# Optimization experiments

Hardware: AMD Instinct MI355X
Metric: run time of the kernel (lower is better)

## Reference

```python
import jax, jax.numpy as jnp
import numpy as np

ATTEN = 8  # atten_size -> window W = 2*ATTEN+1 = 17


def setup_inputs() -> dict:
    key = jax.random.key(0)
    ks = jax.random.split(key, 9)
    B, S, I, H, O = 16, 4096, 64, 64, 2
    xavier = lambda k, fi, fo: jax.random.normal(k, (fi, fo), jnp.float32) * jnp.sqrt(2.0 / (fi + fo))
    return {
        "x": jax.random.normal(ks[0], (B, S, I), jnp.float32),
        "pos_enc": jax.random.normal(ks[1], (B, S, I), jnp.float32),
        "W1": xavier(ks[2], I, H),
        "b1": jnp.zeros((1, 1, H), jnp.float32),
        "Wq": xavier(ks[3], H, H),
        "Wk": xavier(ks[4], H, H),
        "Wv": xavier(ks[5], H, H),
        "W2": xavier(ks[6], H, O),
        "b2": jnp.zeros((1, 1, O), jnp.float32),
    }


def _gather_window(h, a):
    # Replicates pad + roll(k) for k in [-a, a] + stack(dim=2) + slice[a:-a]:
    # x_nei[b, t, j, :] = h[b, t + a - j, :]  (zeros when out of range)
    B, S, H = h.shape
    t = jnp.arange(S)[:, None]
    j = jnp.arange(2 * a + 1)[None, :]
    idx = t + a - j                      # [S, W]
    valid = (idx >= 0) & (idx < S)
    idxc = jnp.clip(idx, 0, S - 1)
    nei = h[:, idxc, :]                  # [B, S, W, H]
    return nei * valid[None, :, :, None].astype(h.dtype)


def reference(x, pos_enc, W1, b1, Wq, Wk, Wv, W2, b2):
    a = ATTEN
    h = x + pos_enc[: x.shape[0]]
    h = jax.nn.relu(h @ W1 + b1)                      # [B, S, H]
    H = h.shape[-1]
    x_nei = _gather_window(h, a)                      # [B, S, W, H]
    q = (h @ Wq)[:, :, None, :]                       # [B, S, 1, H]
    k = x_nei @ Wk                                    # [B, S, W, H]
    v = x_nei @ Wv                                    # [B, S, W, H]
    scores = jnp.einsum("bsoh,bswh->bsow", q, k) / jnp.sqrt(jnp.float32(H))
    # Faithful to torch.nn.Softmax(dim=2) on [B,S,1,W]: softmax over singleton dim -> all ones
    weights = jax.nn.softmax(scores, axis=2)          # [B, S, 1, W]
    att = jnp.einsum("bsow,bswh->bsoh", weights, v)[:, :, 0, :]  # [B, S, H]
    out = att @ W2 + b2                               # [B, S, O]
    return out, weights
```

## Files before the change

kernel.cpp:

```cpp
#include <hip/hip_runtime.h>

#define NB 16
#define NS 4096
#define NTOK (NB * NS)
#define TOKB 64
#define ABLK (NTOK / TOKB)
#define OBLK 256
#define WTS_V ((NB * NS * 17) / 4)

__global__ __launch_bounds__(256, 3) void p_kernel(
    const float* __restrict__ x,
    const float* __restrict__ pe,
    const float* __restrict__ w1p,
    const float* __restrict__ b1p,
    const float* __restrict__ wvp,
    const float* __restrict__ w2p,
    float* __restrict__ pws,
    float* __restrict__ wts)
{
    __shared__ __align__(16) float W1T[64][68];
    __shared__ __align__(16) float XST[64][68];
    __shared__ float MT[2][64];
    __shared__ float B1[64];
    __shared__ float W2S[128];
    __shared__ float PP[16][128];

    const int tid = threadIdx.x;
    const int blk = blockIdx.x;

    const float4* w14 = (const float4*)w1p;
    const float4* xa  = (const float4*)x  + (size_t)blk * (TOKB * 16);
    const float4* pa  = (const float4*)pe + (size_t)blk * (TOKB * 16);
    float4 w1v[4], xv[4], pv[4];
    #pragma unroll
    for (int k = 0; k < 4; ++k) w1v[k] = w14[k * 256 + tid];
    #pragma unroll
    for (int q = 0; q < 4; ++q) xv[q] = xa[q * 256 + tid];
    #pragma unroll
    for (int q = 0; q < 4; ++q) pv[q] = pa[q * 256 + tid];
    if (tid < 128) W2S[tid] = w2p[tid];
    if (tid >= 128 && tid < 192) B1[tid - 128] = b1p[tid - 128];

    #pragma unroll
    for (int k = 0; k < 4; ++k) {
        int f4 = k * 256 + tid;
        int i = f4 >> 4, c = f4 & 15;
        W1T[4*c+0][i] = w1v[k].x;
        W1T[4*c+1][i] = w1v[k].y;
        W1T[4*c+2][i] = w1v[k].z;
        W1T[4*c+3][i] = w1v[k].w;
    }
    #pragma unroll
    for (int q = 0; q < 4; ++q) {
        int f4 = q * 256 + tid;
        int t = f4 >> 4, c = f4 & 15;
        XST[4*c+0][t] = xv[q].x + pv[q].x;
        XST[4*c+1][t] = xv[q].y + pv[q].y;
        XST[4*c+2][t] = xv[q].z + pv[q].z;
        XST[4*c+3][t] = xv[q].w + pv[q].w;
    }
    __syncthreads();

    if (tid < 128) {
        const int o = tid & 1, d = tid >> 1;
        const float4* wv4 = (const float4*)(wvp + (size_t)d * 64);
        float m0 = 0.f, m1 = 0.f, m2 = 0.f, m3 = 0.f;
        #pragma unroll
        for (int j4 = 0; j4 < 16; j4 += 4) {
            float4 a = wv4[j4 + 0], b = wv4[j4 + 1], c = wv4[j4 + 2], e = wv4[j4 + 3];
            int jb = j4 * 4;
            m0 = fmaf(a.x, W2S[(jb+ 0)*2+o], m0); m0 = fmaf(a.y, W2S[(jb+ 1)*2+o], m0);
            m0 = fmaf(a.z, W2S[(jb+ 2)*2+o], m0); m0 = fmaf(a.w, W2S[(jb+ 3)*2+o], m0);
            m1 = fmaf(b.x, W2S[(jb+ 4)*2+o], m1); m1 = fmaf(b.y, W2S[(jb+ 5)*2+o], m1);
            m1 = fmaf(b.z, W2S[(jb+ 6)*2+o], m1); m1 = fmaf(b.w, W2S[(jb+ 7)*2+o], m1);
            m2 = fmaf(c.x, W2S[(jb+ 8)*2+o], m2); m2 = fmaf(c.y, W2S[(jb+ 9)*2+o], m2);
            m2 = fmaf(c.z, W2S[(jb+10)*2+o], m2); m2 = fmaf(c.w, W2S[(jb+11)*2+o], m2);
            m3 = fmaf(e.x, W2S[(jb+12)*2+o], m3); m3 = fmaf(e.y, W2S[(jb+13)*2+o], m3);
            m3 = fmaf(e.z, W2S[(jb+14)*2+o], m3); m3 = fmaf(e.w, W2S[(jb+15)*2+o], m3);
        }
        MT[o][d] = (m0 + m1) + (m2 + m3);
    }
    __syncthreads();

    const int tg = tid & 15;
    const int dg = tid >> 4;
    float4 acc[4];
    #pragma unroll
    for (int dd = 0; dd < 4; ++dd) acc[dd] = make_float4(0.f, 0.f, 0.f, 0.f);

    #pragma unroll 4
    for (int i = 0; i < 64; i += 4) {
        float4 xw0 = *(const float4*)&XST[i + 0][4 * tg];
        float4 xw1 = *(const float4*)&XST[i + 1][4 * tg];
        float4 xw2 = *(const float4*)&XST[i + 2][4 * tg];
        float4 xw3 = *(const float4*)&XST[i + 3][4 * tg];
        #pragma unroll
        for (int dd = 0; dd < 4; ++dd) {
            const float4 w = *(const float4*)&W1T[4 * dg + dd][i];
            acc[dd].x = fmaf(w.x, xw0.x, acc[dd].x);
            acc[dd].y = fmaf(w.x, xw0.y, acc[dd].y);
            acc[dd].z = fmaf(w.x, xw0.z, acc[dd].z);
            acc[dd].w = fmaf(w.x, xw0.w, acc[dd].w);
            acc[dd].x = fmaf(w.y, xw1.x, acc[dd].x);
            acc[dd].y = fmaf(w.y, xw1.y, acc[dd].y);
            acc[dd].z = fmaf(w.y, xw1.z, acc[dd].z);
            acc[dd].w = fmaf(w.y, xw1.w, acc[dd].w);
            acc[dd].x = fmaf(w.z, xw2.x, acc[dd].x);
            acc[dd].y = fmaf(w.z, xw2.y, acc[dd].y);
            acc[dd].z = fmaf(w.z, xw2.z, acc[dd].z);
            acc[dd].w = fmaf(w.z, xw2.w, acc[dd].w);
            acc[dd].x = fmaf(w.w, xw3.x, acc[dd].x);
            acc[dd].y = fmaf(w.w, xw3.y, acc[dd].y);
            acc[dd].z = fmaf(w.w, xw3.z, acc[dd].z);
            acc[dd].w = fmaf(w.w, xw3.w, acc[dd].w);
        }
    }

    float4 p0 = make_float4(0.f,0.f,0.f,0.f), p1 = make_float4(0.f,0.f,0.f,0.f);
    #pragma unroll
    for (int dd = 0; dd < 4; ++dd) {
        const int d = 4 * dg + dd;
        const float bb = B1[d];
        float4 h;
        h.x = fmaxf(acc[dd].x + bb, 0.f);
        h.y = fmaxf(acc[dd].y + bb, 0.f);
        h.z = fmaxf(acc[dd].z + bb, 0.f);
        h.w = fmaxf(acc[dd].w + bb, 0.f);
        const float m0 = MT[0][d], m1 = MT[1][d];
        p0.x = fmaf(h.x, m0, p0.x); p0.y = fmaf(h.y, m0, p0.y);
        p0.z = fmaf(h.z, m0, p0.z); p0.w = fmaf(h.w, m0, p0.w);
        p1.x = fmaf(h.x, m1, p1.x); p1.y = fmaf(h.y, m1, p1.y);
        p1.z = fmaf(h.z, m1, p1.z); p1.w = fmaf(h.w, m1, p1.w);
    }
    *(float2*)&PP[dg][2*(4*tg+0)] = make_float2(p0.x, p1.x);
    *(float2*)&PP[dg][2*(4*tg+1)] = make_float2(p0.y, p1.y);
    *(float2*)&PP[dg][2*(4*tg+2)] = make_float2(p0.z, p1.z);
    *(float2*)&PP[dg][2*(4*tg+3)] = make_float2(p0.w, p1.w);
    __syncthreads();

    if (tid < 128) {
        float s = 0.f;
        #pragma unroll
        for (int g = 0; g < 16; ++g) s += PP[g][tid];
        pws[(size_t)blk * 128 + tid] = s;
    }

    {
        float4* wp = (float4*)wts;
        const float4 one4 = make_float4(1.f, 1.f, 1.f, 1.f);
        for (unsigned idx = (unsigned)blk * 256u + (unsigned)tid;
             idx < WTS_V; idx += (unsigned)ABLK * 256u)
            wp[idx] = one4;
    }
}

__global__ __launch_bounds__(256) void out_kernel(
    const float* __restrict__ pws,
    const float* __restrict__ b2p,
    float* __restrict__ out)
{
    const int g = blockIdx.x * 256 + threadIdx.x;
    const int s = g & (NS - 1);
    const float2* p2 = (const float2*)pws;
    float ax = b2p[0], ay = b2p[1];
    #pragma unroll
    for (int w = -8; w <= 8; ++w) {
        int ss = s + w;
        if (0 <= ss && ss < NS) {
            float2 v = p2[g + w];
            ax += v.x; ay += v.y;
        }
    }
    ((float2*)out)[g] = make_float2(ax, ay);
}

extern "C" void kernel_launch(void* const* d_in, const int* in_sizes, int n_in,
                              void* d_out, int out_size, void* d_ws, size_t ws_size,
                              hipStream_t stream) {
    const float* x  = (const float*)d_in[0];
    const float* pe = (const float*)d_in[1];
    const float* w1 = (const float*)d_in[2];
    const float* b1 = (const float*)d_in[3];
    const float* wv = (const float*)d_in[6];
    const float* w2 = (const float*)d_in[7];
    const float* b2 = (const float*)d_in[8];

    float* out = (float*)d_out;
    float* wts = out + (size_t)NB * NS * 2;
    float* pws = (float*)d_ws;

    p_kernel<<<ABLK, 256, 0, stream>>>(x, pe, w1, b1, wv, w2, pws, wts);
    out_kernel<<<OBLK, 256, 0, stream>>>(pws, b2, out);
}
```

Baseline: 101.5 us.

## Fuse window-sum into single kernel with bf16 MFMA for first projection

Merges the two kernels into one. Each block now handles 128 tokens plus an 8-token halo on each side and computes the 17-wide window sum from shared memory, so the per-token partials no longer round-trip through a workspace buffer and the second launch disappears. The input projection now runs on bf16 MFMA 16x16x32 instructions over swizzled shared-memory fragments, with inputs and weights converted to bf16. The cost is recomputing the halo tokens and losing precision in the first matmul, which could exceed the comparison tolerance.

```diff
diff --git a/kernel.cpp b/kernel.cpp
--- a/kernel.cpp
+++ b/kernel.cpp
@@ -1,69 +1,79 @@
 #include <hip/hip_runtime.h>
 
-#define NB 16
 #define NS 4096
-#define NTOK (NB * NS)
-#define TOKB 64
-#define ABLK (NTOK / TOKB)
-#define OBLK 256
-#define WTS_V ((NB * NS * 17) / 4)
+#define NTOK 65536
+#define TOKB 128
+#define GRID 512
+#define NTILE 9
+#define WTS_V 278528u
+#define F4MAX 1048575
 
-__global__ __launch_bounds__(256, 3) void p_kernel(
-    const float* __restrict__ x,
-    const float* __restrict__ pe,
-    const float* __restrict__ w1p,
-    const float* __restrict__ b1p,
-    const float* __restrict__ wvp,
-    const float* __restrict__ w2p,
-    float* __restrict__ pws,
-    float* __restrict__ wts)
+typedef __attribute__((ext_vector_type(8))) short bfrag;
+typedef __attribute__((ext_vector_type(4))) float f32x4;
+
+__device__ __forceinline__ unsigned short f2bf(float f) {
+    union { unsigned int i; float f; } c; c.f = f;
+    unsigned int u = c.i;
+    unsigned int r = u + 0x7FFFu + ((u >> 16) & 1u);
+    return (unsigned short)(r >> 16);
+}
+
+__global__ __launch_bounds__(256, 2) void fused(
+    const float* __restrict__ x, const float* __restrict__ pe,
+    const float* __restrict__ w1p, const float* __restrict__ b1p,
+    const float* __restrict__ wvp, const float* __restrict__ w2p,
+    const float* __restrict__ b2p,
+    float* __restrict__ out, float* __restrict__ wts)
 {
-    __shared__ __align__(16) float W1T[64][68];
-    __shared__ __align__(16) float XST[64][68];
-    __shared__ float MT[2][64];
-    __shared__ float B1[64];
-    __shared__ float W2S[128];
-    __shared__ float PP[16][128];
+    __shared__ bfrag Xb[144 * 8];
+    __shared__ bfrag Wf[512];
+    __shared__ float B1s[64], M0s[64], M1s[64], W2S[128];
+    __shared__ float PL[146][2];
 
-    const int tid = threadIdx.x;
-    const int blk = blockIdx.x;
+    const int tid  = threadIdx.x;
+    const int blk  = blockIdx.x;
+    const int lane = tid & 63;
+    const int wid  = tid >> 6;
 
-    const float4* w14 = (const float4*)w1p;
-    const float4* xa  = (const float4*)x  + (size_t)blk * (TOKB * 16);
-    const float4* pa  = (const float4*)pe + (size_t)blk * (TOKB * 16);
-    float4 w1v[4], xv[4], pv[4];
+    const int gbase4 = blk * 2048 - 128;
+    const float4* x4 = (const float4*)x;
+    const float4* p4 = (const float4*)pe;
     #pragma unroll
-    for (int k = 0; k < 4; ++k) w1v[k] = w14[k * 256 + tid];
-    #pragma unroll
-    for (int q = 0; q < 4; ++q) xv[q] = xa[q * 256 + tid];
-    #pragma unroll
-    for (int q = 0; q < 4; ++q) pv[q] = pa[q * 256 + tid];
-    if (tid < 128) W2S[tid] = w2p[tid];
-    if (tid >= 128 && tid < 192) B1[tid - 128] = b1p[tid - 128];
-
-    #pragma unroll
-    for (int k = 0; k < 4; ++k) {
-        int f4 = k * 256 + tid;
-        int i = f4 >> 4, c = f4 & 15;
-        W1T[4*c+0][i] = w1v[k].x;
-        W1T[4*c+1][i] = w1v[k].y;
-        W1T[4*c+2][i] = w1v[k].z;
-        W1T[4*c+3][i] = w1v[k].w;
+    for (int it = 0; it < 5; ++it) {
+        int cidx = it * 256 + tid;
+        if (cidx < 1152) {
+            int f0 = gbase4 + cidx * 2, f1 = f0 + 1;
+            f0 = f0 < 0 ? 0 : (f0 > F4MAX ? F4MAX : f0);
+            f1 = f1 < 0 ? 0 : (f1 > F4MAX ? F4MAX : f1);
+            float4 a = x4[f0], b = x4[f1], c = p4[f0], d = p4[f1];
+            union { unsigned short u[8]; bfrag v; } P;
+            P.u[0] = f2bf(a.x + c.x); P.u[1] = f2bf(a.y + c.y);
+            P.u[2] = f2bf(a.z + c.z); P.u[3] = f2bf(a.w + c.w);
+            P.u[4] = f2bf(b.x + d.x); P.u[5] = f2bf(b.y + d.y);
+            P.u[6] = f2bf(b.z + d.z); P.u[7] = f2bf(b.w + d.w);
+            int tl = cidx >> 3;
+            int sc = (cidx & 7) ^ (tl & 7);
+            Xb[tl * 8 + sc] = P.v;
+        }
     }
     #pragma unroll
-    for (int q = 0; q < 4; ++q) {
-        int f4 = q * 256 + tid;
-        int t = f4 >> 4, c = f4 & 15;
-        XST[4*c+0][t] = xv[q].x + pv[q].x;
-        XST[4*c+1][t] = xv[q].y + pv[q].y;
-        XST[4*c+2][t] = xv[q].z + pv[q].z;
-        XST[4*c+3][t] = xv[q].w + pv[q].w;
+    for (int s = 0; s < 2; ++s) {
+        int slot = s * 256 + tid;
+        int kh = slot >> 8, rem = slot & 255, dt = rem >> 6, l = rem & 63;
+        int dd = dt * 16 + (l & 15);
+        int kb = kh * 32 + ((l >> 4) << 3);
+        union { unsigned short u[8]; bfrag v; } P;
+        #pragma unroll
+        for (int j = 0; j < 8; ++j) P.u[j] = f2bf(w1p[(kb + j) * 64 + dd]);
+        Wf[slot] = P.v;
     }
+    if (tid < 64) B1s[tid] = b1p[tid];
+    if (tid >= 64 && tid < 192) W2S[tid - 64] = w2p[tid - 64];
     __syncthreads();
 
     if (tid < 128) {
-        const int o = tid & 1, d = tid >> 1;
-        const float4* wv4 = (const float4*)(wvp + (size_t)d * 64);
+        const int o = tid & 1, dd = tid >> 1;
+        const float4* wv4 = (const float4*)(wvp + (size_t)dd * 64);
         float m0 = 0.f, m1 = 0.f, m2 = 0.f, m3 = 0.f;
         #pragma unroll
         for (int j4 = 0; j4 < 16; j4 += 4) {
@@ -78,100 +88,77 @@
             m3 = fmaf(e.x, W2S[(jb+12)*2+o], m3); m3 = fmaf(e.y, W2S[(jb+13)*2+o], m3);
             m3 = fmaf(e.z, W2S[(jb+14)*2+o], m3); m3 = fmaf(e.w, W2S[(jb+15)*2+o], m3);
         }
-        MT[o][d] = (m0 + m1) + (m2 + m3);
+        float v = (m0 + m1) + (m2 + m3);
+        if (o) M1s[dd] = v; else M0s[dd] = v;
     }
     __syncthreads();
 
-    const int tg = tid & 15;
-    const int dg = tid >> 4;
-    float4 acc[4];
+    const int cl = lane & 15;
+    float biasv[4], m0v[4], m1v[4];
     #pragma unroll
-    for (int dd = 0; dd < 4; ++dd) acc[dd] = make_float4(0.f, 0.f, 0.f, 0.f);
-
-    #pragma unroll 4
-    for (int i = 0; i < 64; i += 4) {
-        float4 xw0 = *(const float4*)&XST[i + 0][4 * tg];
-        float4 xw1 = *(const float4*)&XST[i + 1][4 * tg];
-        float4 xw2 = *(const float4*)&XST[i + 2][4 * tg];
-        float4 xw3 = *(const float4*)&XST[i + 3][4 * tg];
+    for (int dt = 0; dt < 4; ++dt) {
+        biasv[dt] = B1s[dt * 16 + cl];
+        m0v[dt]   = M0s[dt * 16 + cl];
+        m1v[dt]   = M1s[dt * 16 + cl];
+    }
+    const int sbase = (blk & 31) * 128 - 8;
+    for (int tau = wid; tau < NTILE; tau += 4) {
+        float pr0[4] = {0.f,0.f,0.f,0.f}, pr1[4] = {0.f,0.f,0.f,0.f};
+        const int arow = (tau * 16 + cl) * 8;
         #pragma unroll
-        for (int dd = 0; dd < 4; ++dd) {
-            const float4 w = *(const float4*)&W1T[4 * dg + dd][i];
-            acc[dd].x = fmaf(w.x, xw0.x, acc[dd].x);
-            acc[dd].y = fmaf(w.x, xw0.y, acc[dd].y);
-            acc[dd].z = fmaf(w.x, xw0.z, acc[dd].z);
-            acc[dd].w = fmaf(w.x, xw0.w, acc[dd].w);
-            acc[dd].x = fmaf(w.y, xw1.x, acc[dd].x);
-            acc[dd].y = fmaf(w.y, xw1.y, acc[dd].y);
-            acc[dd].z = fmaf(w.y, xw1.z, acc[dd].z);
-            acc[dd].w = fmaf(w.y, xw1.w, acc[dd].w);
-            acc[dd].x = fmaf(w.z, xw2.x, acc[dd].x);
-            acc[dd].y = fmaf(w.z, xw2.y, acc[dd].y);
-            acc[dd].z = fmaf(w.z, xw2.z, acc[dd].z);
-            acc[dd].w = fmaf(w.z, xw2.w, acc[dd].w);
-            acc[dd].x = fmaf(w.w, xw3.x, acc[dd].x);
-            acc[dd].y = fmaf(w.w, xw3.y, acc[dd].y);
-            acc[dd].z = fmaf(w.w, xw3.z, acc[dd].z);
-            acc[dd].w = fmaf(w.w, xw3.w, acc[dd].w);
+        for (int dt = 0; dt < 4; ++dt) {
+            f32x4 acc = {0.f, 0.f, 0.f, 0.f};
+            #pragma unroll
+            for (int kh = 0; kh < 2; ++kh) {
+                bfrag av = Xb[arow + (((kh << 2) + (lane >> 4)) ^ (lane & 7))];
+                bfrag bv = Wf[(kh * 4 + dt) * 64 + lane];
+                acc = __builtin_amdgcn_mfma_f32_16x16x32_bf16(av, bv, acc, 0, 0, 0);
+            }
+            #pragma unroll
+            for (int rg = 0; rg < 4; ++rg) {
+                float h = fmaxf(acc[rg] + biasv[dt], 0.f);
+                pr0[rg] = fmaf(h, m0v[dt], pr0[rg]);
+                pr1[rg] = fmaf(h, m1v[dt], pr1[rg]);
+            }
+        }
+        #pragma unroll
+        for (int rg = 0; rg < 4; ++rg) {
+            #pragma unroll
+            for (int m = 1; m < 16; m <<= 1) {
+                pr0[rg] += __shfl_xor(pr0[rg], m);
+                pr1[rg] += __shfl_xor(pr1[rg], m);
+            }
+        }
+        if ((lane & 15) == 0) {
+            const int rgrp = lane >> 4;
+            #pragma unroll
+            for (int rg = 0; rg < 4; ++rg) {
+                int tl = tau * 16 + rgrp * 4 + rg;
+                bool valid = (unsigned)(sbase + tl) < 4096u;
+                PL[tl][0] = valid ? pr0[rg] : 0.f;
+                PL[tl][1] = valid ? pr1[rg] : 0.f;
+            }
         }
     }
-
-    float4 p0 = make_float4(0.f,0.f,0.f,0.f), p1 = make_float4(0.f,0.f,0.f,0.f);
-    #pragma unroll
-    for (int dd = 0; dd < 4; ++dd) {
-        const int d = 4 * dg + dd;
-        const float bb = B1[d];
-        float4 h;
-        h.x = fmaxf(acc[dd].x + bb, 0.f);
-        h.y = fmaxf(acc[dd].y + bb, 0.f);
-        h.z = fmaxf(acc[dd].z + bb, 0.f);
-        h.w = fmaxf(acc[dd].w + bb, 0.f);
-        const float m0 = MT[0][d], m1 = MT[1][d];
-        p0.x = fmaf(h.x, m0, p0.x); p0.y = fmaf(h.y, m0, p0.y);
-        p0.z = fmaf(h.z, m0, p0.z); p0.w = fmaf(h.w, m0, p0.w);
-        p1.x = fmaf(h.x, m1, p1.x); p1.y = fmaf(h.y, m1, p1.y);
-        p1.z = fmaf(h.z, m1, p1.z); p1.w = fmaf(h.w, m1, p1.w);
-    }
-    *(float2*)&PP[dg][2*(4*tg+0)] = make_float2(p0.x, p1.x);
-    *(float2*)&PP[dg][2*(4*tg+1)] = make_float2(p0.y, p1.y);
-    *(float2*)&PP[dg][2*(4*tg+2)] = make_float2(p0.z, p1.z);
-    *(float2*)&PP[dg][2*(4*tg+3)] = make_float2(p0.w, p1.w);
     __syncthreads();
 
     if (tid < 128) {
-        float s = 0.f;
+        float ax = b2p[0], ay = b2p[1];
         #pragma unroll
-        for (int g = 0; g < 16; ++g) s += PP[g][tid];
-        pws[(size_t)blk * 128 + tid] = s;
+        for (int k = 0; k <= 16; ++k) {
+            float2 v = *(const float2*)&PL[tid + k][0];
+            ax += v.x; ay += v.y;
+        }
+        ((float2*)out)[(size_t)blk * 128 + tid] = make_float2(ax, ay);
     }
 
     {
         float4* wp = (float4*)wts;
         const float4 one4 = make_float4(1.f, 1.f, 1.f, 1.f);
         for (unsigned idx = (unsigned)blk * 256u + (unsigned)tid;
-             idx < WTS_V; idx += (unsigned)ABLK * 256u)
+             idx < WTS_V; idx += (unsigned)GRID * 256u)
             wp[idx] = one4;
     }
-}
-
-__global__ __launch_bounds__(256) void out_kernel(
-    const float* __restrict__ pws,
-    const float* __restrict__ b2p,
-    float* __restrict__ out)
-{
-    const int g = blockIdx.x * 256 + threadIdx.x;
-    const int s = g & (NS - 1);
-    const float2* p2 = (const float2*)pws;
-    float ax = b2p[0], ay = b2p[1];
-    #pragma unroll
-    for (int w = -8; w <= 8; ++w) {
-        int ss = s + w;
-        if (0 <= ss && ss < NS) {
-            float2 v = p2[g + w];
-            ax += v.x; ay += v.y;
-        }
-    }
-    ((float2*)out)[g] = make_float2(ax, ay);
 }
 
 extern "C" void kernel_launch(void* const* d_in, const int* in_sizes, int n_in,
@@ -186,9 +173,7 @@
     const float* b2 = (const float*)d_in[8];
 
     float* out = (float*)d_out;
-    float* wts = out + (size_t)NB * NS * 2;
-    float* pws = (float*)d_ws;
+    float* wts = out + (size_t)NTOK * 2;
 
-    p_kernel<<<ABLK, 256, 0, stream>>>(x, pe, w1, b1, wv, w2, pws, wts);
-    out_kernel<<<OBLK, 256, 0, stream>>>(pws, b2, out);
+    fused<<<GRID, 256, 0, stream>>>(x, pe, w1, b1, wv, w2, b2, out, wts);
 }
```

Measured after the change: 93.71 us. 7.7% less time.
